# Performance work log

Measured on AMD Instinct MI355X. Metric: run time of the kernel, lower is better.

Reference implementation:

```python
import jax, jax.numpy as jnp
import numpy as np

PI = 3.141592653589
RMAX = 6.0
RMIN = 0.5
NBASIS = 25
B, NATOM, MNBR = 8, 256, 100


def setup_inputs() -> dict:
    key = jax.random.key(0)
    ks = jax.random.split(key, 10)
    Imagetype = jax.random.randint(ks[0], (B, NATOM), 1, 5)
    neighbor_list = jax.random.randint(ks[1], (B, NATOM, MNBR), 0, NATOM + 1)
    # rij in (0.2, 7.0): some neighbors fall outside the 6.0 cutoff
    r = jax.random.uniform(ks[2], (B, NATOM, MNBR), minval=0.2, maxval=7.0)
    xyz = jax.random.normal(ks[3], (B, NATOM, MNBR, 3))
    xyz = xyz / (jnp.linalg.norm(xyz, axis=-1, keepdims=True) + 1e-6) * r[..., None]
    ImagedR = jnp.concatenate([r[..., None], xyz], axis=-1)  # [B,N,M,4]
    n_embed = 0.1 + 0.2 * jax.random.normal(ks[4], (40, 5))
    W1 = 0.04 * jax.random.normal(ks[5], (100, 625)); b1 = jnp.zeros((100,))
    W2 = 0.10 * jax.random.normal(ks[6], (100, 100)); b2 = jnp.zeros((100,))
    W3 = 0.10 * jax.random.normal(ks[7], (100, 100)); b3 = jnp.zeros((100,))
    W4 = 0.10 * jax.random.normal(ks[8], (1, 100)); b4 = 3.3 + jax.random.normal(ks[9], (1,))
    return dict(Imagetype=Imagetype, neighbor_list=neighbor_list, ImagedR=ImagedR,
                n_embed=n_embed, W1=W1, b1=b1, W2=W2, b2=b2, W3=W3, b3=b3, W4=W4, b4=b4)


def _moment(ImagedR):
    # radial basis fc and its analytic d(fc)/dr projected onto x,y,z directions
    rij = ImagedR[..., 0]            # [B,N,M]
    xyz = ImagedR[..., 1:4]          # [B,N,M,3]
    rs = jnp.linspace(RMIN, RMAX, NBASIS)
    r = rij[..., None]               # [B,N,M,1] broadcast vs rs -> [B,N,M,25]
    cond = (r < RMAX) & (r > 0)
    gauss = jnp.exp(-(r - rs) ** 2)
    cut = 0.5 * jnp.cos(PI * r) + 0.5
    fc = jnp.where(cond, gauss * cut, 0.0)
    dfc = jnp.where(cond, gauss * (-2.0 * (r - rs)) * cut - gauss * 0.5 * PI * jnp.sin(PI * r), 0.0)
    unit = jnp.where(rij[..., None] != 0, xyz / rij[..., None], 0.0)   # [B,N,M,3]
    dfeat = unit[:, :, :, None, :] * dfc[..., None]                    # [B,N,M,25,3]
    return fc, dfeat


def _energy(feat, Imagetype, neighbor_list, n_embed, W1, b1, W2, b2, W3, b3, W4, b4):
    b, n, m, k = feat.shape
    # type of each neighbor; index 0 (no neighbor) -> type 0
    padded = jnp.concatenate([jnp.zeros((b, 1), Imagetype.dtype), Imagetype], axis=1)  # [B,N+1]
    nbr_type = padded[jnp.arange(b)[:, None, None], neighbor_list]                     # [B,N,M]
    iit = n_embed[Imagetype]        # [B,N,5]
    jjt = n_embed[nbr_type]         # [B,N,M,5]
    emb = (iit[:, :, None, :, None] * jjt[:, :, :, None, :]).reshape(b, n, m, 25)
    # outer(feat_k, emb_e) summed over neighbors -> [B,N,25,25]
    G = jnp.einsum('bnmk,bnme->bnke', feat, emb).reshape(b, n, 625)
    x1 = G @ W1.T + b1
    x3 = jnp.tanh(x1) @ W2.T + b2 + x1
    x5 = jnp.tanh(x3) @ W3.T + b3 + x3
    Ei = jnp.tanh(x5) @ W4.T + b4   # [B,N,1]
    Etot = Ei.sum(axis=1)           # [B,1]
    return Etot, Ei


def reference(Imagetype, neighbor_list, ImagedR, n_embed, W1, b1, W2, b2, W3, b3, W4, b4):
    b, n, m = neighbor_list.shape
    feat, dfeat = _moment(ImagedR)
    Etot, Ei = _energy(feat, Imagetype, neighbor_list, n_embed, W1, b1, W2, b2, W3, b3, W4, b4)
    # dE/dfeat with ones cotangent on Etot (== grad of sum)
    dE = jax.grad(lambda f: _energy(f, Imagetype, neighbor_list, n_embed,
                                    W1, b1, W2, b2, W3, b3, W4, b4)[0].sum())(feat)  # [B,N,M,25]
    dE_Rid = jnp.einsum('bnmk,bnmkd->bnmd', dE, dfeat)  # [B,N,M,3]
    Force = -dE_Rid.sum(axis=2)                         # [B,N,3]
    # scatter-add reaction forces onto neighbor atoms (1-based ids, 0 = padding)
    buf = jnp.zeros((b, n + 1, 3), dE_Rid.dtype).at[
        jnp.arange(b)[:, None, None], neighbor_list].add(dE_Rid)
    Force = Force + buf[:, 1:]
    return Etot, Ei, Force
```

## Files before the change

kernel.cpp:

```cpp
#include <hip/hip_runtime.h>
#include <math.h>

#define PI_F 3.14159274f
#define STEP (5.5f/24.0f)

constexpr int BATCH = 8;
constexpr int NATOM = 256;
constexpr int MNBR  = 100;
constexpr int NB    = 25;
constexpr int NATOT = BATCH * NATOM;
constexpr int NPBLK = 256;

constexpr int OFF_W1T  = 0;
constexpr int OFF_W1TT = 62500;
constexpr int OFF_W2T  = 125000;
constexpr int OFF_W3T  = 135000;
constexpr int OFF_H    = 145000;
constexpr int OFF_PART = 145000 + 2048 * 125;
constexpr size_t WS_NEED = (size_t)(OFF_PART + NPBLK * 768) * 4;

__global__ __launch_bounds__(256)
void k_feat(const int* __restrict__ itype, const int* __restrict__ nbr,
            const float* __restrict__ imdR, const float* __restrict__ nemb,
            const float* __restrict__ W1, const float* __restrict__ W2,
            const float* __restrict__ W3, float* __restrict__ ws)
{
    int atom = blockIdx.x;
    int b    = atom >> 8;
    int tid  = threadIdx.x;

    if (blockIdx.x < 500) {
        int t = blockIdx.x / 100, jo = blockIdx.x - (blockIdx.x / 100) * 100;
        if (tid < 125) {
            int k = tid / 5, j = tid - k * 5;
            float s = 0.f;
            #pragma unroll
            for (int i = 0; i < 5; i++)
                s = fmaf(W1[jo * 625 + k * 25 + i * 5 + j], nemb[t * 5 + i], s);
            ws[OFF_W1T  + (t * 100 + jo) * 125 + tid] = s;
            ws[OFF_W1TT + (t * 125 + tid) * 100 + jo] = s;
        }
    } else if (blockIdx.x < 600) {
        int jo = blockIdx.x - 500;
        if (tid < 100) {
            ws[OFF_W2T + tid * 100 + jo] = W2[jo * 100 + tid];
            ws[OFF_W3T + tid * 100 + jo] = W3[jo * 100 + tid];
        }
    }

    __shared__ float r_s[MNBR], cut_s[MNBR];
    __shared__ float jjt_s[MNBR * 5];
    __shared__ float feat_s[MNBR * NB];
    __shared__ float Hp_s[2][128];

    if (tid < MNBR) {
        int m = tid;
        float4 v = *reinterpret_cast<const float4*>(imdR + ((size_t)atom * MNBR + m) * 4);
        float r = v.x;
        r_s[m]   = r;
        cut_s[m] = 0.5f * cosf(PI_F * r) + 0.5f;
        int j  = nbr[atom * MNBR + m];
        int tj = (j > 0) ? itype[b * NATOM + (j - 1)] : 0;
        #pragma unroll
        for (int q = 0; q < 5; q++) jjt_s[m * 5 + q] = nemb[tj * 5 + q];
    }
    __syncthreads();

    for (int w = tid; w < MNBR * NB; w += 256) {
        int m = w / NB, k = w - m * NB;
        float r = r_s[m];
        float d = r - (0.5f + k * STEP);
        float g = expf(-d * d);
        float fc = (r < 6.0f && r > 0.0f) ? g * cut_s[m] : 0.0f;
        feat_s[m * NB + k] = fc;
    }
    __syncthreads();

    if (tid < 250) {
        int h = tid / 125, o = tid - h * 125;
        int k = o / 5, j = o - (o / 5) * 5;
        float acc = 0.f;
        for (int m = h * 50; m < h * 50 + 50; m++)
            acc = fmaf(feat_s[m * NB + k], jjt_s[m * 5 + j], acc);
        Hp_s[h][o] = acc;
    }
    __syncthreads();
    if (tid < 125)
        ws[OFF_H + (size_t)atom * 125 + tid] = Hp_s[0][tid] + Hp_s[1][tid];
}

__global__ __launch_bounds__(512)
void k_mlp(const int* __restrict__ itype,
           const float* __restrict__ b1, const float* __restrict__ W2,
           const float* __restrict__ b2, const float* __restrict__ W3,
           const float* __restrict__ b3, const float* __restrict__ W4,
           const float* __restrict__ b4,
           float* __restrict__ ws, float* __restrict__ out)
{
    int base = blockIdx.x * 4;
    int tid  = threadIdx.x;

    __shared__ float H_s[4 * 125];
    __shared__ float x1_s[400], t1_s[400], x3_s[400], t3_s[400], t5_s[400];
    __shared__ float g5_s[400], g3_s[400], g1_s[400];
    __shared__ int   t_s[4];

    if (tid < 4) t_s[tid] = itype[base + tid];
    if (tid < 500) H_s[tid] = ws[OFF_H + (size_t)base * 125 + tid];
    __syncthreads();

    if (tid < 400) {
        int a = tid / 100, jo = tid - (tid / 100) * 100;
        const float* wt = ws + OFF_W1TT + t_s[a] * 12500;
        const float* hh = H_s + a * 125;
        float acc = 0.f;
        for (int q = 0; q < 125; q++)
            acc = fmaf(wt[q * 100 + jo], hh[q], acc);
        float v = acc + b1[jo];
        x1_s[tid] = v; t1_s[tid] = tanhf(v);
    }
    __syncthreads();

    if (tid < 400) {
        int a = tid / 100, jo = tid - (tid / 100) * 100;
        const float* wt = ws + OFF_W2T;
        const float* tt = t1_s + a * 100;
        float acc = 0.f;
        for (int k = 0; k < 100; k++) acc = fmaf(wt[k * 100 + jo], tt[k], acc);
        float v = acc + b2[jo] + x1_s[tid];
        x3_s[tid] = v; t3_s[tid] = tanhf(v);
    }
    __syncthreads();

    if (tid < 400) {
        int a = tid / 100, jo = tid - (tid / 100) * 100;
        const float* wt = ws + OFF_W3T;
        const float* tt = t3_s + a * 100;
        float acc = 0.f;
        for (int k = 0; k < 100; k++) acc = fmaf(wt[k * 100 + jo], tt[k], acc);
        float v = acc + b3[jo] + x3_s[tid];
        t5_s[tid] = tanhf(v);
    }
    __syncthreads();

    if (tid < 256) {
        int a = tid >> 6, lane = tid & 63;
        float acc = 0.f;
        for (int j = lane; j < 100; j += 64) acc += t5_s[a * 100 + j] * W4[j];
        #pragma unroll
        for (int mm = 32; mm > 0; mm >>= 1) acc += __shfl_xor(acc, mm, 64);
        if (lane == 0) out[8 + base + a] = acc + b4[0];
    }

    if (tid < 400) {
        int jo = tid - (tid / 100) * 100;
        float t = t5_s[tid];
        g5_s[tid] = W4[jo] * (1.f - t * t);
    }
    __syncthreads();

    if (tid < 400) {
        int a = tid / 100, k = tid - (tid / 100) * 100;
        const float* gg = g5_s + a * 100;
        float acc = 0.f;
        for (int j = 0; j < 100; j++) acc = fmaf(W3[j * 100 + k], gg[j], acc);
        float t = t3_s[tid];
        g3_s[tid] = g5_s[tid] + (1.f - t * t) * acc;
    }
    __syncthreads();

    if (tid < 400) {
        int a = tid / 100, k = tid - (tid / 100) * 100;
        const float* gg = g3_s + a * 100;
        float acc = 0.f;
        for (int j = 0; j < 100; j++) acc = fmaf(W2[j * 100 + k], gg[j], acc);
        float t = t1_s[tid];
        g1_s[tid] = g3_s[tid] + (1.f - t * t) * acc;
    }
    __syncthreads();

    if (tid < 500) {
        int a = tid / 125, q = tid - (tid / 125) * 125;
        const float* wt = ws + OFF_W1T + t_s[a] * 12500;
        const float* gg = g1_s + a * 100;
        float acc = 0.f;
        for (int jo = 0; jo < 100; jo++)
            acc = fmaf(wt[jo * 125 + q], gg[jo], acc);
        ws[OFF_H + (size_t)(base + a) * 125 + q] = acc;
    }
}

template<bool USE_PART>
__global__ __launch_bounds__(512)
void k_bwd(const int* __restrict__ itype, const int* __restrict__ nbr,
           const float* __restrict__ imdR, const float* __restrict__ nemb,
           float* __restrict__ ws, float* __restrict__ out)
{
    int bid = blockIdx.x;
    int tid = threadIdx.x;
    int w   = tid >> 6, lane = tid & 63;
    int atom = bid * 8 + w;
    int b    = atom >> 8;

    __shared__ float dH_s[8][128];
    __shared__ float fbuf[NATOM * 3];

    for (int q = tid; q < NATOM * 3; q += 512) fbuf[q] = 0.f;

    const float* dhp = ws + OFF_H + (size_t)atom * 125;
    for (int o = lane; o < 125; o += 64) dH_s[w][o] = dhp[o];
    __syncthreads();

    float sf0 = 0.f, sf1 = 0.f, sf2 = 0.f;
    #pragma unroll
    for (int mh = 0; mh < 2; mh++) {
        int m = lane * 2 + mh;
        if (m < MNBR) {
            float4 v = *reinterpret_cast<const float4*>(imdR + ((size_t)atom * MNBR + m) * 4);
            float r = v.x;
            float sc, cc; sincosf(PI_F * r, &sc, &cc);
            float cut = 0.5f * cc + 0.5f;
            float sterm = 0.5f * PI_F * sc;
            int j = nbr[atom * MNBR + m];
            int tj = (j > 0) ? itype[b * NATOM + (j - 1)] : 0;
            float j0 = nemb[tj*5+0], j1 = nemb[tj*5+1], j2 = nemb[tj*5+2],
                  j3 = nemb[tj*5+3], j4 = nemb[tj*5+4];
            float s = 0.f;
            for (int k = 0; k < NB; k++) {
                const float* dh = &dH_s[w][k * 5];
                float dE = j0*dh[0] + j1*dh[1] + j2*dh[2] + j3*dh[3] + j4*dh[4];
                float d  = r - (0.5f + k * STEP);
                float g  = expf(-d * d);
                float dfc = g * (-2.f * d) * cut - g * sterm;
                s = fmaf(dE, dfc, s);
            }
            if (!(r < 6.0f && r > 0.0f)) s = 0.f;
            float inv = (r != 0.f) ? 1.f / r : 0.f;
            float d0 = s * v.y * inv, d1 = s * v.z * inv, d2 = s * v.w * inv;
            sf0 += d0; sf1 += d1; sf2 += d2;
            if (j > 0) {
                atomicAdd(&fbuf[(j - 1) * 3 + 0], d0);
                atomicAdd(&fbuf[(j - 1) * 3 + 1], d1);
                atomicAdd(&fbuf[(j - 1) * 3 + 2], d2);
            }
        }
    }
    #pragma unroll
    for (int mm = 32; mm > 0; mm >>= 1) {
        sf0 += __shfl_xor(sf0, mm, 64);
        sf1 += __shfl_xor(sf1, mm, 64);
        sf2 += __shfl_xor(sf2, mm, 64);
    }
    if (lane == 0) {
        int tl = atom & 255;
        atomicAdd(&fbuf[tl * 3 + 0], -sf0);
        atomicAdd(&fbuf[tl * 3 + 1], -sf1);
        atomicAdd(&fbuf[tl * 3 + 2], -sf2);
    }
    __syncthreads();

    if (USE_PART) {
        for (int q = tid; q < NATOM * 3; q += 512)
            ws[OFF_PART + (size_t)bid * 768 + q] = fbuf[q];
    } else {
        for (int q = tid; q < NATOM * 3; q += 512) {
            float vq = fbuf[q];
            if (vq != 0.f) atomicAdd(&out[8 + NATOT + (b << 8) * 3 + q], vq);
        }
    }
}

__global__ __launch_bounds__(256)
void k_red(const float* __restrict__ ws, float* __restrict__ out, int nfblk)
{
    int bid = blockIdx.x, tid = threadIdx.x;
    if (bid < nfblk) {
        int idx = bid * 256 + tid;
        int b = idx / 768, q = idx - b * 768;
        float s = 0.f;
        #pragma unroll 4
        for (int p = 0; p < 32; p++)
            s += ws[OFF_PART + (size_t)(b * 32 + p) * 768 + q];
        out[8 + NATOT + idx] = s;
    } else {
        int e = bid - nfblk;
        float v = out[8 + e * 256 + tid];
        #pragma unroll
        for (int mm = 32; mm > 0; mm >>= 1) v += __shfl_xor(v, mm, 64);
        __shared__ float wsum[4];
        if ((tid & 63) == 0) wsum[tid >> 6] = v;
        __syncthreads();
        if (tid == 0) out[e] = wsum[0] + wsum[1] + wsum[2] + wsum[3];
    }
}

extern "C" void kernel_launch(void* const* d_in, const int* in_sizes, int n_in,
                              void* d_out, int out_size, void* d_ws, size_t ws_size,
                              hipStream_t stream)
{
    (void)in_sizes; (void)n_in;

    const int*   itype = (const int*)  d_in[0];
    const int*   nbr   = (const int*)  d_in[1];
    const float* imdR  = (const float*)d_in[2];
    const float* nemb  = (const float*)d_in[3];
    const float* W1    = (const float*)d_in[4];
    const float* b1    = (const float*)d_in[5];
    const float* W2    = (const float*)d_in[6];
    const float* b2    = (const float*)d_in[7];
    const float* W3    = (const float*)d_in[8];
    const float* b3    = (const float*)d_in[9];
    const float* W4    = (const float*)d_in[10];
    const float* b4    = (const float*)d_in[11];

    float* out = (float*)d_out;
    float* ws  = (float*)d_ws;

    bool use_part = ws_size >= WS_NEED;
    if (!use_part)
        hipMemsetAsync((char*)d_out + (size_t)(8 + NATOT) * 4, 0,
                       (size_t)NATOT * 3 * 4, stream);

    hipLaunchKernelGGL(k_feat, dim3(NATOT), dim3(256), 0, stream,
                       itype, nbr, imdR, nemb, W1, W2, W3, ws);
    hipLaunchKernelGGL(k_mlp, dim3(NATOT / 4), dim3(512), 0, stream,
                       itype, b1, W2, b2, W3, b3, W4, b4, ws, out);
    if (use_part) {
        hipLaunchKernelGGL((k_bwd<true>), dim3(NPBLK), dim3(512), 0, stream,
                           itype, nbr, imdR, nemb, ws, out);
        hipLaunchKernelGGL(k_red, dim3(32), dim3(256), 0, stream, ws, out, 24);
    } else {
        hipLaunchKernelGGL((k_bwd<false>), dim3(NPBLK), dim3(512), 0, stream,
                           itype, nbr, imdR, nemb, ws, out);
        hipLaunchKernelGGL(k_red, dim3(8), dim3(256), 0, stream, ws, out, 0);
    }
}
```

Before: 131.5 us.

## Fuse feature, MLP and backward force kernels into one per-4-atom kernel

Merges the feature, MLP forward/backward and force-backprop kernels into a single kernel that handles 4 atoms per block. The per-atom H and dH vectors and the neighbor geometry stay in shared memory, which removes the global round-trips and two launches. Backward matvecs now read the transposed W2/W3 copies from the workspace, giving contiguous per-thread rows. In exchange there are more partial force buffers (512 blocks × 768 floats) for the reduction kernel to sum, and larger per-block shared memory that may lower occupancy.

```diff
diff --git a/kernel.cpp b/kernel.cpp
--- a/kernel.cpp
+++ b/kernel.cpp
@@ -9,104 +9,101 @@
 constexpr int MNBR  = 100;
 constexpr int NB    = 25;
 constexpr int NATOT = BATCH * NATOM;
-constexpr int NPBLK = 256;
+constexpr int ABLK  = 4;
+constexpr int NMBLK = NATOT / ABLK;
+constexpr int PPB   = NMBLK / BATCH;
 
 constexpr int OFF_W1T  = 0;
 constexpr int OFF_W1TT = 62500;
 constexpr int OFF_W2T  = 125000;
 constexpr int OFF_W3T  = 135000;
-constexpr int OFF_H    = 145000;
-constexpr int OFF_PART = 145000 + 2048 * 125;
-constexpr size_t WS_NEED = (size_t)(OFF_PART + NPBLK * 768) * 4;
-
-__global__ __launch_bounds__(256)
-void k_feat(const int* __restrict__ itype, const int* __restrict__ nbr,
-            const float* __restrict__ imdR, const float* __restrict__ nemb,
-            const float* __restrict__ W1, const float* __restrict__ W2,
-            const float* __restrict__ W3, float* __restrict__ ws)
+constexpr int OFF_PART = 145000;
+constexpr size_t WS_NEED = (size_t)(OFF_PART + NMBLK * 768) * 4;
+
+__global__ __launch_bounds__(128)
+void k_prep(const float* __restrict__ nemb, const float* __restrict__ W1,
+            const float* __restrict__ W2, const float* __restrict__ W3,
+            float* __restrict__ ws)
 {
-    int atom = blockIdx.x;
-    int b    = atom >> 8;
-    int tid  = threadIdx.x;
-
-    if (blockIdx.x < 500) {
-        int t = blockIdx.x / 100, jo = blockIdx.x - (blockIdx.x / 100) * 100;
+    int bid = blockIdx.x, tid = threadIdx.x;
+    if (bid < 500) {
+        int t = bid / 100, jo = bid - (bid / 100) * 100;
         if (tid < 125) {
-            int k = tid / 5, j = tid - k * 5;
+            int k = tid / 5, j = tid - (tid / 5) * 5;
             float s = 0.f;
             #pragma unroll
             for (int i = 0; i < 5; i++)
                 s = fmaf(W1[jo * 625 + k * 25 + i * 5 + j], nemb[t * 5 + i], s);
             ws[OFF_W1T  + (t * 100 + jo) * 125 + tid] = s;
-            ws[OFF_W1TT + (t * 125 + tid) * 100 + jo] = s;
-        }
-    } else if (blockIdx.x < 600) {
-        int jo = blockIdx.x - 500;
+            ws[OFF_W1TT + t * 12500 + tid * 100 + jo] = s;
+        }
+    } else {
+        int jo = bid - 500;
         if (tid < 100) {
             ws[OFF_W2T + tid * 100 + jo] = W2[jo * 100 + tid];
             ws[OFF_W3T + tid * 100 + jo] = W3[jo * 100 + tid];
         }
     }
-
-    __shared__ float r_s[MNBR], cut_s[MNBR];
-    __shared__ float jjt_s[MNBR * 5];
-    __shared__ float feat_s[MNBR * NB];
-    __shared__ float Hp_s[2][128];
-
-    if (tid < MNBR) {
-        int m = tid;
+}
+
+template<bool USE_PART>
+__global__ __launch_bounds__(512)
+void k_main(const int* __restrict__ itype, const int* __restrict__ nbr,
+            const float* __restrict__ imdR, const float* __restrict__ nemb,
+            const float* __restrict__ b1, const float* __restrict__ b2,
+            const float* __restrict__ b3, const float* __restrict__ W4,
+            const float* __restrict__ b4,
+            float* __restrict__ ws, float* __restrict__ out)
+{
+    int base = blockIdx.x * ABLK;
+    int b    = base >> 8;
+    int tid  = threadIdx.x;
+
+    __shared__ float r_s[400], cut_s[400], sin_s[400];
+    __shared__ float x_s[400], y_s[400], z_s[400];
+    __shared__ int   nb_s[400];
+    __shared__ float jjt_s[2000];
+    __shared__ float H_s[500];
+    __shared__ float x1_s[400], t1_s[400], x3_s[400], t3_s[400], t5_s[400];
+    __shared__ float g5_s[400], g3_s[400], g1_s[400];
+    __shared__ float fbuf[NATOM * 3];
+    __shared__ int   t_s[4];
+
+    if (tid < 4) t_s[tid] = itype[base + tid];
+    for (int q = tid; q < NATOM * 3; q += 512) fbuf[q] = 0.f;
+    if (tid < 400) {
+        int a = tid / 100, m = tid - (tid / 100) * 100;
+        int atom = base + a;
         float4 v = *reinterpret_cast<const float4*>(imdR + ((size_t)atom * MNBR + m) * 4);
         float r = v.x;
-        r_s[m]   = r;
-        cut_s[m] = 0.5f * cosf(PI_F * r) + 0.5f;
-        int j  = nbr[atom * MNBR + m];
+        r_s[tid] = r;
+        float sc, cc; sincosf(PI_F * r, &sc, &cc);
+        bool cond = (r < 6.0f && r > 0.0f);
+        cut_s[tid] = cond ? (0.5f * cc + 0.5f) : 0.f;
+        sin_s[tid] = cond ? sc : 0.f;
+        x_s[tid] = v.y; y_s[tid] = v.z; z_s[tid] = v.w;
+        int j = nbr[atom * MNBR + m];
+        nb_s[tid] = j;
         int tj = (j > 0) ? itype[b * NATOM + (j - 1)] : 0;
         #pragma unroll
-        for (int q = 0; q < 5; q++) jjt_s[m * 5 + q] = nemb[tj * 5 + q];
-    }
-    __syncthreads();
-
-    for (int w = tid; w < MNBR * NB; w += 256) {
-        int m = w / NB, k = w - m * NB;
-        float r = r_s[m];
-        float d = r - (0.5f + k * STEP);
-        float g = expf(-d * d);
-        float fc = (r < 6.0f && r > 0.0f) ? g * cut_s[m] : 0.0f;
-        feat_s[m * NB + k] = fc;
-    }
-    __syncthreads();
-
-    if (tid < 250) {
-        int h = tid / 125, o = tid - h * 125;
-        int k = o / 5, j = o - (o / 5) * 5;
-        float acc = 0.f;
-        for (int m = h * 50; m < h * 50 + 50; m++)
-            acc = fmaf(feat_s[m * NB + k], jjt_s[m * 5 + j], acc);
-        Hp_s[h][o] = acc;
-    }
-    __syncthreads();
-    if (tid < 125)
-        ws[OFF_H + (size_t)atom * 125 + tid] = Hp_s[0][tid] + Hp_s[1][tid];
-}
-
-__global__ __launch_bounds__(512)
-void k_mlp(const int* __restrict__ itype,
-           const float* __restrict__ b1, const float* __restrict__ W2,
-           const float* __restrict__ b2, const float* __restrict__ W3,
-           const float* __restrict__ b3, const float* __restrict__ W4,
-           const float* __restrict__ b4,
-           float* __restrict__ ws, float* __restrict__ out)
-{
-    int base = blockIdx.x * 4;
-    int tid  = threadIdx.x;
-
-    __shared__ float H_s[4 * 125];
-    __shared__ float x1_s[400], t1_s[400], x3_s[400], t3_s[400], t5_s[400];
-    __shared__ float g5_s[400], g3_s[400], g1_s[400];
-    __shared__ int   t_s[4];
-
-    if (tid < 4) t_s[tid] = itype[base + tid];
-    if (tid < 500) H_s[tid] = ws[OFF_H + (size_t)base * 125 + tid];
+        for (int q = 0; q < 5; q++) jjt_s[tid * 5 + q] = nemb[tj * 5 + q];
+    }
+    __syncthreads();
+
+    if (tid < 500) {
+        int a = tid / 125, q = tid - (tid / 125) * 125;
+        int k = q / 5, j = q - (q / 5) * 5;
+        float rs = 0.5f + k * STEP;
+        int am0 = a * 100;
+        float acc = 0.f;
+        for (int m = 0; m < MNBR; m++) {
+            float r = r_s[am0 + m];
+            float d = r - rs;
+            float g = expf(-d * d);
+            acc = fmaf(g * cut_s[am0 + m], jjt_s[(am0 + m) * 5 + j], acc);
+        }
+        H_s[tid] = acc;
+    }
     __syncthreads();
 
     if (tid < 400) {
@@ -114,8 +111,7 @@
         const float* wt = ws + OFF_W1TT + t_s[a] * 12500;
         const float* hh = H_s + a * 125;
         float acc = 0.f;
-        for (int q = 0; q < 125; q++)
-            acc = fmaf(wt[q * 100 + jo], hh[q], acc);
+        for (int q = 0; q < 125; q++) acc = fmaf(wt[q * 100 + jo], hh[q], acc);
         float v = acc + b1[jo];
         x1_s[tid] = v; t1_s[tid] = tanhf(v);
     }
@@ -151,7 +147,6 @@
         for (int mm = 32; mm > 0; mm >>= 1) acc += __shfl_xor(acc, mm, 64);
         if (lane == 0) out[8 + base + a] = acc + b4[0];
     }
-
     if (tid < 400) {
         int jo = tid - (tid / 100) * 100;
         float t = t5_s[tid];
@@ -162,8 +157,9 @@
     if (tid < 400) {
         int a = tid / 100, k = tid - (tid / 100) * 100;
         const float* gg = g5_s + a * 100;
-        float acc = 0.f;
-        for (int j = 0; j < 100; j++) acc = fmaf(W3[j * 100 + k], gg[j], acc);
+        const float* wt = ws + OFF_W3T + k * 100;
+        float acc = 0.f;
+        for (int j = 0; j < 100; j++) acc = fmaf(wt[j], gg[j], acc);
         float t = t3_s[tid];
         g3_s[tid] = g5_s[tid] + (1.f - t * t) * acc;
     }
@@ -172,8 +168,9 @@
     if (tid < 400) {
         int a = tid / 100, k = tid - (tid / 100) * 100;
         const float* gg = g3_s + a * 100;
-        float acc = 0.f;
-        for (int j = 0; j < 100; j++) acc = fmaf(W2[j * 100 + k], gg[j], acc);
+        const float* wt = ws + OFF_W2T + k * 100;
+        float acc = 0.f;
+        for (int j = 0; j < 100; j++) acc = fmaf(wt[j], gg[j], acc);
         float t = t1_s[tid];
         g1_s[tid] = g3_s[tid] + (1.f - t * t) * acc;
     }
@@ -184,84 +181,58 @@
         const float* wt = ws + OFF_W1T + t_s[a] * 12500;
         const float* gg = g1_s + a * 100;
         float acc = 0.f;
-        for (int jo = 0; jo < 100; jo++)
-            acc = fmaf(wt[jo * 125 + q], gg[jo], acc);
-        ws[OFF_H + (size_t)(base + a) * 125 + q] = acc;
-    }
-}
-
-template<bool USE_PART>
-__global__ __launch_bounds__(512)
-void k_bwd(const int* __restrict__ itype, const int* __restrict__ nbr,
-           const float* __restrict__ imdR, const float* __restrict__ nemb,
-           float* __restrict__ ws, float* __restrict__ out)
-{
-    int bid = blockIdx.x;
-    int tid = threadIdx.x;
-    int w   = tid >> 6, lane = tid & 63;
-    int atom = bid * 8 + w;
-    int b    = atom >> 8;
-
-    __shared__ float dH_s[8][128];
-    __shared__ float fbuf[NATOM * 3];
-
-    for (int q = tid; q < NATOM * 3; q += 512) fbuf[q] = 0.f;
-
-    const float* dhp = ws + OFF_H + (size_t)atom * 125;
-    for (int o = lane; o < 125; o += 64) dH_s[w][o] = dhp[o];
-    __syncthreads();
-
-    float sf0 = 0.f, sf1 = 0.f, sf2 = 0.f;
-    #pragma unroll
-    for (int mh = 0; mh < 2; mh++) {
-        int m = lane * 2 + mh;
-        if (m < MNBR) {
-            float4 v = *reinterpret_cast<const float4*>(imdR + ((size_t)atom * MNBR + m) * 4);
-            float r = v.x;
-            float sc, cc; sincosf(PI_F * r, &sc, &cc);
-            float cut = 0.5f * cc + 0.5f;
-            float sterm = 0.5f * PI_F * sc;
-            int j = nbr[atom * MNBR + m];
-            int tj = (j > 0) ? itype[b * NATOM + (j - 1)] : 0;
-            float j0 = nemb[tj*5+0], j1 = nemb[tj*5+1], j2 = nemb[tj*5+2],
-                  j3 = nemb[tj*5+3], j4 = nemb[tj*5+4];
+        for (int jo = 0; jo < 100; jo++) acc = fmaf(wt[jo * 125 + q], gg[jo], acc);
+        H_s[tid] = acc;
+    }
+    __syncthreads();
+
+    {
+        int w = tid >> 6, lane = tid & 63;
+        int a = w >> 1, h = w & 1;
+        float d0 = 0.f, d1 = 0.f, d2 = 0.f;
+        if (lane < 50) {
+            int am = a * 100 + h * 50 + lane;
+            float r = r_s[am], cut = cut_s[am];
+            float sterm = 0.5f * PI_F * sin_s[am];
+            float j0 = jjt_s[am*5+0], j1v = jjt_s[am*5+1], j2 = jjt_s[am*5+2],
+                  j3 = jjt_s[am*5+3], j4 = jjt_s[am*5+4];
+            const float* dh0 = H_s + a * 125;
             float s = 0.f;
             for (int k = 0; k < NB; k++) {
-                const float* dh = &dH_s[w][k * 5];
-                float dE = j0*dh[0] + j1*dh[1] + j2*dh[2] + j3*dh[3] + j4*dh[4];
+                const float* dh = dh0 + k * 5;
+                float dE = j0*dh[0] + j1v*dh[1] + j2*dh[2] + j3*dh[3] + j4*dh[4];
                 float d  = r - (0.5f + k * STEP);
                 float g  = expf(-d * d);
                 float dfc = g * (-2.f * d) * cut - g * sterm;
                 s = fmaf(dE, dfc, s);
             }
-            if (!(r < 6.0f && r > 0.0f)) s = 0.f;
             float inv = (r != 0.f) ? 1.f / r : 0.f;
-            float d0 = s * v.y * inv, d1 = s * v.z * inv, d2 = s * v.w * inv;
-            sf0 += d0; sf1 += d1; sf2 += d2;
+            d0 = s * x_s[am] * inv; d1 = s * y_s[am] * inv; d2 = s * z_s[am] * inv;
+            int j = nb_s[am];
             if (j > 0) {
                 atomicAdd(&fbuf[(j - 1) * 3 + 0], d0);
                 atomicAdd(&fbuf[(j - 1) * 3 + 1], d1);
                 atomicAdd(&fbuf[(j - 1) * 3 + 2], d2);
             }
         }
-    }
-    #pragma unroll
-    for (int mm = 32; mm > 0; mm >>= 1) {
-        sf0 += __shfl_xor(sf0, mm, 64);
-        sf1 += __shfl_xor(sf1, mm, 64);
-        sf2 += __shfl_xor(sf2, mm, 64);
-    }
-    if (lane == 0) {
-        int tl = atom & 255;
-        atomicAdd(&fbuf[tl * 3 + 0], -sf0);
-        atomicAdd(&fbuf[tl * 3 + 1], -sf1);
-        atomicAdd(&fbuf[tl * 3 + 2], -sf2);
+        #pragma unroll
+        for (int mm = 32; mm > 0; mm >>= 1) {
+            d0 += __shfl_xor(d0, mm, 64);
+            d1 += __shfl_xor(d1, mm, 64);
+            d2 += __shfl_xor(d2, mm, 64);
+        }
+        if (lane == 0) {
+            int tl = (base + a) & 255;
+            atomicAdd(&fbuf[tl * 3 + 0], -d0);
+            atomicAdd(&fbuf[tl * 3 + 1], -d1);
+            atomicAdd(&fbuf[tl * 3 + 2], -d2);
+        }
     }
     __syncthreads();
 
     if (USE_PART) {
         for (int q = tid; q < NATOM * 3; q += 512)
-            ws[OFF_PART + (size_t)bid * 768 + q] = fbuf[q];
+            ws[OFF_PART + (size_t)blockIdx.x * 768 + q] = fbuf[q];
     } else {
         for (int q = tid; q < NATOM * 3; q += 512) {
             float vq = fbuf[q];
@@ -278,9 +249,9 @@
         int idx = bid * 256 + tid;
         int b = idx / 768, q = idx - b * 768;
         float s = 0.f;
-        #pragma unroll 4
-        for (int p = 0; p < 32; p++)
-            s += ws[OFF_PART + (size_t)(b * 32 + p) * 768 + q];
+        #pragma unroll 8
+        for (int p = 0; p < PPB; p++)
+            s += ws[OFF_PART + (size_t)(b * PPB + p) * 768 + q];
         out[8 + NATOT + idx] = s;
     } else {
         int e = bid - nfblk;
@@ -321,17 +292,15 @@
         hipMemsetAsync((char*)d_out + (size_t)(8 + NATOT) * 4, 0,
                        (size_t)NATOT * 3 * 4, stream);
 
-    hipLaunchKernelGGL(k_feat, dim3(NATOT), dim3(256), 0, stream,
-                       itype, nbr, imdR, nemb, W1, W2, W3, ws);
-    hipLaunchKernelGGL(k_mlp, dim3(NATOT / 4), dim3(512), 0, stream,
-                       itype, b1, W2, b2, W3, b3, W4, b4, ws, out);
+    hipLaunchKernelGGL(k_prep, dim3(600), dim3(128), 0, stream,
+                       nemb, W1, W2, W3, ws);
     if (use_part) {
-        hipLaunchKernelGGL((k_bwd<true>), dim3(NPBLK), dim3(512), 0, stream,
-                           itype, nbr, imdR, nemb, ws, out);
+        hipLaunchKernelGGL((k_main<true>), dim3(NMBLK), dim3(512), 0, stream,
+                           itype, nbr, imdR, nemb, b1, b2, b3, W4, b4, ws, out);
         hipLaunchKernelGGL(k_red, dim3(32), dim3(256), 0, stream, ws, out, 24);
     } else {
-        hipLaunchKernelGGL((k_bwd<false>), dim3(NPBLK), dim3(512), 0, stream,
-                           itype, nbr, imdR, nemb, ws, out);
+        hipLaunchKernelGGL((k_main<false>), dim3(NMBLK), dim3(512), 0, stream,
+                           itype, nbr, imdR, nemb, b1, b2, b3, W4, b4, ws, out);
         hipLaunchKernelGGL(k_red, dim3(8), dim3(256), 0, stream, ws, out, 0);
     }
 }
```

Measured after the change: 136.5 us. +3.8%, slower.
